# Optimization experiments

Measured on AMD Instinct MI355X. Metric: run time of the kernel, lower is better.

## Reference

```python
import jax, jax.numpy as jnp
import numpy as np

B, N, C = 2, 2048, 768
H = 12
HD = C // H  # 64


def setup_inputs() -> dict:
    key = jax.random.key(0)
    ks = jax.random.split(key, 6)
    s = 0.02
    x = jax.random.normal(ks[0], (B, N, C), dtype=jnp.float32)
    xpos = jnp.arange(B * N, dtype=jnp.int64).reshape(B, N) % N
    W_qkv = jax.random.normal(ks[1], (3 * C, C), dtype=jnp.float32) * s
    b_qkv = jnp.zeros((3 * C,), dtype=jnp.float32)
    W_proj = jax.random.normal(ks[2], (C, C), dtype=jnp.float32) * s
    b_proj = jnp.zeros((C,), dtype=jnp.float32)
    return {"x": x, "xpos": xpos, "W_qkv": W_qkv, "b_qkv": b_qkv,
            "W_proj": W_proj, "b_proj": b_proj}


def reference(x, xpos, W_qkv, b_qkv, W_proj, b_proj):
    # rope is None in this configuration -> xpos is unused, matching torch module.
    Bx, Nx, Cx = x.shape
    scale = (Cx // H) ** -0.5
    qkv = x @ W_qkv.T + b_qkv                     # [B, N, 3C]
    qkv = qkv.reshape(Bx, Nx, 3, H, HD)
    q = jnp.einsum('bnhd->bhnd', qkv[:, :, 0])    # [B, H, N, HD]
    k = jnp.einsum('bnhd->bhnd', qkv[:, :, 1])
    v = jnp.einsum('bnhd->bhnd', qkv[:, :, 2])
    attn = jnp.einsum('bhnd,bhmd->bhnm', q, k) * scale  # [B, H, N, N]
    attn = jax.nn.softmax(attn, axis=-1)
    out = jnp.einsum('bhnm,bhmd->bhnd', attn, v)  # [B, H, N, HD]
    out = jnp.einsum('bhnd->bnhd', out).reshape(Bx, Nx, Cx)
    return out @ W_proj.T + b_proj
```

## Files before the change

kernel.cpp:

```cpp
#include <hip/hip_runtime.h>
#include <hip/hip_bf16.h>


typedef _Float16 half8 __attribute__((ext_vector_type(8)));
typedef _Float16 half4_t __attribute__((ext_vector_type(4)));
typedef float floatx4 __attribute__((ext_vector_type(4)));
typedef float floatx16 __attribute__((ext_vector_type(16)));
typedef unsigned int uintx4 __attribute__((ext_vector_type(4)));
typedef unsigned int uintx2 __attribute__((ext_vector_type(2)));

#define SCALE_LOG2E 0.1803368801111204f

constexpr int XH_OFF    = 0;
constexpr int WQKV_OFF  = XH_OFF + 4096 * 768;
constexpr int WPROJ_OFF = WQKV_OFF + 2304 * 768;
constexpr int QK_OFF    = WPROJ_OFF + 768 * 768;
constexpr int VTH_OFF   = QK_OFF + 4096 * 1536;
constexpr int PO_OFF    = VTH_OFF + 24 * 64 * 2048;
constexpr int PSTAT_OFF = PO_OFF + 2 * 24 * 2048 * 64;

__device__ __forceinline__ void gl16(const _Float16* g, _Float16* l) {
  __builtin_amdgcn_global_load_lds(
      (const __attribute__((address_space(1))) unsigned int*)g,
      (__attribute__((address_space(3))) unsigned int*)l, 16, 0, 0);
}

__global__ __launch_bounds__(256) void cvt_all(const float* __restrict__ x,
                                               const float* __restrict__ wqkv,
                                               const float* __restrict__ wproj,
                                               _Float16* __restrict__ ws) {
  constexpr int n1 = 4096 * 768 / 4;
  constexpr int n2 = 2304 * 768 / 4;
  int i = blockIdx.x * 256 + threadIdx.x;
  const float* src; _Float16* dst; int j;
  if (i < n1)           { src = x;     dst = ws + XH_OFF;    j = i; }
  else if (i < n1 + n2) { src = wqkv;  dst = ws + WQKV_OFF;  j = i - n1; }
  else                  { src = wproj; dst = ws + WPROJ_OFF; j = i - n1 - n2; }
  floatx4 f = *(const floatx4*)(src + 4 * j);
  half4_t h;
  h[0] = (_Float16)f[0]; h[1] = (_Float16)f[1];
  h[2] = (_Float16)f[2]; h[3] = (_Float16)f[3];
  *(half4_t*)(dst + 4 * j) = h;
}

__global__ __launch_bounds__(256) void qkv_gemm(const _Float16* __restrict__ xh,
                                                const _Float16* __restrict__ wh,
                                                const float* __restrict__ bias,
                                                _Float16* __restrict__ qkh,
                                                _Float16* __restrict__ vth) {
  __shared__ __align__(16) _Float16 sA[128 * 64];
  __shared__ __align__(16) _Float16 sB[128 * 64];
  const int tid = threadIdx.x;
  const int nblk = blockIdx.x % 18, mblk = blockIdx.x / 18;
  const int lane = tid & 63, w = tid >> 6;
  const int q31 = lane & 31, hi = lane >> 5;
  const int lrow = lane >> 3;
  const int lchunk = (lane & 7) ^ lrow;
  const int wq = w >> 1, wn = w & 1;

  floatx16 acc[2][2];
#pragma unroll
  for (int mr = 0; mr < 2; ++mr)
#pragma unroll
    for (int nc = 0; nc < 2; ++nc)
#pragma unroll
      for (int i = 0; i < 16; ++i) acc[mr][nc][i] = 0.f;

  for (int kt = 0; kt < 12; ++kt) {
    if (kt) __syncthreads();
#pragma unroll
    for (int i = 0; i < 8; ++i) {
      int g = i * 32 + w * 8;
      if (g < 128)
        gl16(xh + (mblk * 128 + g + lrow) * 768 + kt * 64 + lchunk * 8, sA + g * 64);
      else
        gl16(wh + (nblk * 128 + (g - 128) + lrow) * 768 + kt * 64 + lchunk * 8,
             sB + (g - 128) * 64);
    }
    __syncthreads();
#pragma unroll
    for (int c = 0; c < 4; ++c) {
      half8 af[2], bf[2];
#pragma unroll
      for (int mr = 0; mr < 2; ++mr) {
        int row = wq * 64 + mr * 32 + q31;
        af[mr] = *(const half8*)(sA + row * 64 + (((c * 2 + hi) ^ (row & 7)) * 8));
      }
#pragma unroll
      for (int nc = 0; nc < 2; ++nc) {
        int row = wn * 64 + nc * 32 + q31;
        bf[nc] = *(const half8*)(sB + row * 64 + (((c * 2 + hi) ^ (row & 7)) * 8));
      }
#pragma unroll
      for (int mr = 0; mr < 2; ++mr)
#pragma unroll
        for (int nc = 0; nc < 2; ++nc)
          acc[mr][nc] = __builtin_amdgcn_mfma_f32_32x32x16_f16(af[mr], bf[nc], acc[mr][nc], 0, 0, 0);
    }
  }

#pragma unroll
  for (int mr = 0; mr < 2; ++mr) {
    const int tok0 = mblk * 128 + wq * 64 + mr * 32;
#pragma unroll
    for (int nc = 0; nc < 2; ++nc) {
      int cbase = nblk * 128 + wn * 64 + nc * 32;
      int col = cbase + q31;
      float bv = bias[col];
      if (cbase < 1536) {
        float sc = (cbase < 768) ? SCALE_LOG2E : 1.0f;
#pragma unroll
        for (int r = 0; r < 16; ++r) {
          int token = tok0 + (r & 3) + 8 * (r >> 2) + 4 * hi;
          qkh[token * 1536 + col] = (_Float16)((acc[mr][nc][r] + bv) * sc);
        }
      } else {
        int dcol = cbase - 1536 + q31;
        int h = dcol >> 6, d = dcol & 63;
        int bh = (tok0 >> 11) * 12 + h;
#pragma unroll
        for (int g2 = 0; g2 < 4; ++g2) {
          int n0 = (tok0 & 2047) + g2 * 8 + hi * 4;
          half4_t hv;
#pragma unroll
          for (int e = 0; e < 4; ++e) hv[e] = (_Float16)(acc[mr][nc][g2 * 4 + e] + bv);
          *(half4_t*)(vth + (bh * 64 + d) * 2048 + n0) = hv;
        }
      }
    }
  }
}

__global__ __launch_bounds__(256, 4) void attn_fused(const _Float16* __restrict__ qkh,
                                                     const _Float16* __restrict__ vth,
                                                     _Float16* __restrict__ pO,
                                                     float* __restrict__ pL) {
  __shared__ __align__(16) _Float16 sK[2][64 * 64];
  __shared__ __align__(16) _Float16 sVT[2][64 * 64];
  const int tid = threadIdx.x;
  const int bx = blockIdx.x;
  const int bh = bx % 24;
  const int rest = bx / 24;
  const int ks = rest & 1, qt = rest >> 1;
  const int b = bh / 12, h = bh % 12;
  const int lane = tid & 63, w = tid >> 6;
  const int q = lane & 31, hi = lane >> 5;

  const int qkbase = b * 2048 * 1536 + h * 64;
  const int qrow = qt * 128 + w * 32 + q;

  half8 qf[4];
#pragma unroll
  for (int c = 0; c < 4; ++c)
    qf[c] = *(const half8*)(qkh + qkbase + qrow * 1536 + c * 16 + hi * 8);

  const int l3 = lane >> 3;
  const int lc = (lane & 7) ^ l3;
  const int key0 = ks * 1024;
  const _Float16* kbase = qkh + qkbase + 768 + (key0 + w * 8 + l3) * 1536 + lc * 8;
  const _Float16* vbase = vth + (bh * 64 + w * 8 + l3) * 2048 + key0 + lc * 8;

  floatx16 O[2];
#pragma unroll
  for (int dg = 0; dg < 2; ++dg)
#pragma unroll
    for (int i = 0; i < 16; ++i) O[dg][i] = 0.f;
  float lrow = 0.f;

  auto stage = [&](int kt, int bufsel) {
    _Float16* dK = (_Float16*)sK[bufsel] + w * 512;
    _Float16* dV = (_Float16*)sVT[bufsel] + w * 512;
    const _Float16* kc = kbase + kt * 64 * 1536;
    const _Float16* vc = vbase + kt * 64;
    gl16(kc, dK);
    gl16(kc + 32 * 1536, dK + 2048);
    gl16(vc, dV);
    gl16(vc + 32 * 2048, dV + 2048);
  };

  stage(0, 0);

  for (int kt = 0; kt < 16; ++kt) {
    __syncthreads();
    if (kt < 15) stage(kt + 1, (kt + 1) & 1);
    const _Float16* cK = &sK[kt & 1][0];
    const _Float16* cV = &sVT[kt & 1][0];

    float rsum = 0.f;
#pragma unroll
    for (int og = 0; og < 2; ++og) {
      floatx16 s;
#pragma unroll
      for (int i = 0; i < 16; ++i) s[i] = 0.f;
      const int krow = og * 32 + q;
#pragma unroll
      for (int c = 0; c < 4; ++c) {
        half8 kf = *(const half8*)(cK + krow * 64 + (((c * 2 + hi) ^ (krow & 7)) * 8));
        s = __builtin_amdgcn_mfma_f32_32x32x16_f16(kf, qf[c], s, 0, 0, 0);
      }

#pragma unroll
      for (int mm = 0; mm < 2; ++mm) {
        const int rb = mm * 8;
        float e0 = __builtin_amdgcn_exp2f(s[rb + 0]);
        float e1 = __builtin_amdgcn_exp2f(s[rb + 1]);
        float e2 = __builtin_amdgcn_exp2f(s[rb + 2]);
        float e3 = __builtin_amdgcn_exp2f(s[rb + 3]);
        float e4 = __builtin_amdgcn_exp2f(s[rb + 4]);
        float e5 = __builtin_amdgcn_exp2f(s[rb + 5]);
        float e6 = __builtin_amdgcn_exp2f(s[rb + 6]);
        float e7 = __builtin_amdgcn_exp2f(s[rb + 7]);
        rsum += ((e0 + e1) + (e2 + e3)) + ((e4 + e5) + (e6 + e7));
        unsigned ua = __builtin_bit_cast(unsigned, __builtin_amdgcn_cvt_pkrtz(e0, e1));
        unsigned ub = __builtin_bit_cast(unsigned, __builtin_amdgcn_cvt_pkrtz(e2, e3));
        unsigned uc = __builtin_bit_cast(unsigned, __builtin_amdgcn_cvt_pkrtz(e4, e5));
        unsigned ud = __builtin_bit_cast(unsigned, __builtin_amdgcn_cvt_pkrtz(e6, e7));
        uintx2 sAC = __builtin_amdgcn_permlane32_swap(ua, uc, false, false);
        uintx2 sBD = __builtin_amdgcn_permlane32_swap(ub, ud, false, false);
        uintx4 u; u[0] = sAC[0]; u[1] = sBD[0]; u[2] = sAC[1]; u[3] = sBD[1];
        half8 bfrag = __builtin_bit_cast(half8, u);

        const int rc2 = (og * 2 + mm) * 2 + hi;
#pragma unroll
        for (int dg = 0; dg < 2; ++dg) {
          const int vrow = dg * 32 + q;
          half8 vf = *(const half8*)(cV + vrow * 64 + ((rc2 ^ (vrow & 7)) * 8));
          O[dg] = __builtin_amdgcn_mfma_f32_32x32x16_f16(vf, bfrag, O[dg], 0, 0, 0);
        }
      }
    }
    lrow += rsum;
  }

  const int prow = (ks * 24 + bh) * 2048 + qt * 128 + w * 32;
#pragma unroll
  for (int dg = 0; dg < 2; ++dg)
#pragma unroll
    for (int g2 = 0; g2 < 4; ++g2) {
      half4_t hv;
#pragma unroll
      for (int e = 0; e < 4; ++e) hv[e] = (_Float16)O[dg][g2 * 4 + e];
      *(half4_t*)(pO + (prow + q) * 64 + dg * 32 + g2 * 8 + hi * 4) = hv;
    }
  lrow += __shfl_xor(lrow, 32, 64);
  if (lane < 32) pL[prow + lane] = lrow;
}

__global__ __launch_bounds__(256) void proj_gemm(const _Float16* __restrict__ pO,
                                                 const float* __restrict__ pL,
                                                 const _Float16* __restrict__ wh,
                                                 const float* __restrict__ bias,
                                                 float* __restrict__ out) {
  __shared__ __align__(16) _Float16 sA[64 * 64];
  __shared__ __align__(16) _Float16 sB[128 * 64];
  const int tid = threadIdx.x;
  const int nblk = blockIdx.x % 6, mblk = blockIdx.x / 6;
  const int lane = tid & 63, w = tid >> 6;
  const int q31 = lane & 31, hi = lane >> 5;
  const int lrow = lane >> 3;
  const int lchunk = (lane & 7) ^ lrow;
  const int wq = w >> 1, wn = w & 1;
  const int arow = tid >> 2, achk = tid & 3;
  const int tok0 = mblk * 64;
  const int b = tok0 >> 11, tokl = tok0 & 2047;

  floatx16 acc[2];
#pragma unroll
  for (int nc = 0; nc < 2; ++nc)
#pragma unroll
    for (int i = 0; i < 16; ++i) acc[nc][i] = 0.f;

  for (int kt = 0; kt < 12; ++kt) {
    const int bh = b * 12 + kt;
    const int row1 = bh * 2048 + tokl + arow;
    const int row2 = (24 + bh) * 2048 + tokl + arow;
    float f = 1.0f / (pL[row1] + pL[row2]);

    if (kt) __syncthreads();
#pragma unroll
    for (int i = 0; i < 4; ++i) {
      int g = i * 32 + w * 8;
      gl16(wh + (nblk * 128 + g + lrow) * 768 + kt * 64 + lchunk * 8, sB + g * 64);
    }
#pragma unroll
    for (int cc = 0; cc < 2; ++cc) {
      int c8 = achk + 4 * cc;
      half8 o1 = *(const half8*)(pO + row1 * 64 + c8 * 8);
      half8 o2 = *(const half8*)(pO + row2 * 64 + c8 * 8);
      half8 o;
#pragma unroll
      for (int e = 0; e < 8; ++e)
        o[e] = (_Float16)(f * ((float)o1[e] + (float)o2[e]));
      *(half8*)(sA + arow * 64 + ((c8 ^ (arow & 7)) * 8)) = o;
    }
    __syncthreads();

#pragma unroll
    for (int c = 0; c < 4; ++c) {
      const int arow2 = wq * 32 + q31;
      half8 af = *(const half8*)(sA + arow2 * 64 + (((c * 2 + hi) ^ (arow2 & 7)) * 8));
      half8 bf[2];
#pragma unroll
      for (int nc = 0; nc < 2; ++nc) {
        int row = wn * 64 + nc * 32 + q31;
        bf[nc] = *(const half8*)(sB + row * 64 + (((c * 2 + hi) ^ (row & 7)) * 8));
      }
#pragma unroll
      for (int nc = 0; nc < 2; ++nc)
        acc[nc] = __builtin_amdgcn_mfma_f32_32x32x16_f16(af, bf[nc], acc[nc], 0, 0, 0);
    }
  }

  const int mtok0 = mblk * 64 + wq * 32;
#pragma unroll
  for (int nc = 0; nc < 2; ++nc) {
    int col = nblk * 128 + wn * 64 + nc * 32 + q31;
    float bv = bias[col];
#pragma unroll
    for (int r = 0; r < 16; ++r) {
      int token = mtok0 + (r & 3) + 8 * (r >> 2) + 4 * hi;
      out[token * 768 + col] = acc[nc][r] + bv;
    }
  }
}

extern "C" void kernel_launch(void* const* d_in, const int* in_sizes, int n_in,
                              void* d_out, int out_size, void* d_ws, size_t ws_size,
                              hipStream_t stream) {
  const float* x     = (const float*)d_in[0];
  const float* wqkv  = (const float*)d_in[2];
  const float* bqkv  = (const float*)d_in[3];
  const float* wproj = (const float*)d_in[4];
  const float* bproj = (const float*)d_in[5];
  float* out = (float*)d_out;

  _Float16* ws = (_Float16*)d_ws;
  _Float16* xh     = ws + XH_OFF;
  _Float16* wqkvh  = ws + WQKV_OFF;
  _Float16* wprojh = ws + WPROJ_OFF;
  _Float16* qkh    = ws + QK_OFF;
  _Float16* vth    = ws + VTH_OFF;
  _Float16* pO     = ws + PO_OFF;
  float*    pL     = (float*)(ws + PSTAT_OFF);

  constexpr int total_v4 = (4096 * 768 + 2304 * 768 + 768 * 768) / 4;
  cvt_all<<<total_v4 / 256, 256, 0, stream>>>(x, wqkv, wproj, ws);
  qkv_gemm<<<32 * 18, 256, 0, stream>>>(xh, wqkvh, bqkv, qkh, vth);
  attn_fused<<<24 * 32, 256, 0, stream>>>(qkh, vth, pO, pL);
  proj_gemm<<<64 * 6, 256, 0, stream>>>(pO, pL, wprojh, bproj, out);
}
```

Before: 166.7 us.

## Double-buffer QKV GEMM LDS tiles and use explicit vmcnt waits with raw barriers

The QKV GEMM now keeps two LDS buffers and issues global-to-LDS loads for the next K tile before computing the current one. This is meant to hide global load latency behind MFMA work. In both the GEMM and the attention loop, __syncthreads is replaced by a raw s_barrier plus a partial s_waitcnt vmcnt, so the next tile's loads can stay in flight. The risk is a race: each wave waits only for its own loads after the barrier, so it may read LDS rows that other waves have not finished writing.

```diff
diff --git a/kernel.cpp b/kernel.cpp
--- a/kernel.cpp
+++ b/kernel.cpp
@@ -48,8 +48,8 @@
                                                 const float* __restrict__ bias,
                                                 _Float16* __restrict__ qkh,
                                                 _Float16* __restrict__ vth) {
-  __shared__ __align__(16) _Float16 sA[128 * 64];
-  __shared__ __align__(16) _Float16 sB[128 * 64];
+  __shared__ __align__(16) _Float16 sA[2][128 * 64];
+  __shared__ __align__(16) _Float16 sB[2][128 * 64];
   const int tid = threadIdx.x;
   const int nblk = blockIdx.x % 18, mblk = blockIdx.x / 18;
   const int lane = tid & 63, w = tid >> 6;
@@ -66,30 +66,43 @@
 #pragma unroll
       for (int i = 0; i < 16; ++i) acc[mr][nc][i] = 0.f;
 
-  for (int kt = 0; kt < 12; ++kt) {
-    if (kt) __syncthreads();
+  auto stage = [&](int kt, int sel) {
 #pragma unroll
     for (int i = 0; i < 8; ++i) {
       int g = i * 32 + w * 8;
       if (g < 128)
-        gl16(xh + (mblk * 128 + g + lrow) * 768 + kt * 64 + lchunk * 8, sA + g * 64);
+        gl16(xh + (mblk * 128 + g + lrow) * 768 + kt * 64 + lchunk * 8,
+             &sA[sel][g * 64]);
       else
         gl16(wh + (nblk * 128 + (g - 128) + lrow) * 768 + kt * 64 + lchunk * 8,
-             sB + (g - 128) * 64);
-    }
-    __syncthreads();
+             &sB[sel][(g - 128) * 64]);
+    }
+  };
+
+  stage(0, 0);
+
+  for (int kt = 0; kt < 12; ++kt) {
+    __builtin_amdgcn_s_barrier();
+    if (kt < 11) {
+      stage(kt + 1, (kt + 1) & 1);
+      asm volatile("s_waitcnt vmcnt(8)" ::: "memory");
+    } else {
+      asm volatile("s_waitcnt vmcnt(0)" ::: "memory");
+    }
+    const _Float16* cA = sA[kt & 1];
+    const _Float16* cB = sB[kt & 1];
 #pragma unroll
     for (int c = 0; c < 4; ++c) {
       half8 af[2], bf[2];
 #pragma unroll
       for (int mr = 0; mr < 2; ++mr) {
         int row = wq * 64 + mr * 32 + q31;
-        af[mr] = *(const half8*)(sA + row * 64 + (((c * 2 + hi) ^ (row & 7)) * 8));
+        af[mr] = *(const half8*)(cA + row * 64 + (((c * 2 + hi) ^ (row & 7)) * 8));
       }
 #pragma unroll
       for (int nc = 0; nc < 2; ++nc) {
         int row = wn * 64 + nc * 32 + q31;
-        bf[nc] = *(const half8*)(sB + row * 64 + (((c * 2 + hi) ^ (row & 7)) * 8));
+        bf[nc] = *(const half8*)(cB + row * 64 + (((c * 2 + hi) ^ (row & 7)) * 8));
       }
 #pragma unroll
       for (int mr = 0; mr < 2; ++mr)
@@ -181,8 +194,13 @@
   stage(0, 0);
 
   for (int kt = 0; kt < 16; ++kt) {
-    __syncthreads();
-    if (kt < 15) stage(kt + 1, (kt + 1) & 1);
+    __builtin_amdgcn_s_barrier();
+    if (kt < 15) {
+      stage(kt + 1, (kt + 1) & 1);
+      asm volatile("s_waitcnt vmcnt(4)" ::: "memory");
+    } else {
+      asm volatile("s_waitcnt vmcnt(0)" ::: "memory");
+    }
     const _Float16* cK = &sK[kt & 1][0];
     const _Float16* cV = &sVT[kt & 1][0];
 
```

Result: slower. 170.4 us (+2.2%).
